# Optimization experiments

Hardware: AMD Instinct MI355X
Metric: run time of the kernel (lower is better)

Reference implementation:

```python
import jax, jax.numpy as jnp
import numpy as np

_J6 = jnp.array([[0, 0, 0, 0, 0, 1], [0, 0, 0, 0, -1, 0], [0, 0, 0, 1, 0, 0],
                 [0, 0, 1, 0, 0, 0], [0, -1, 0, 0, 0, 0], [1, 0, 0, 0, 0, 0]], dtype=jnp.float32)
_PAIRS4 = [(0, 1), (0, 2), (0, 3), (1, 2), (1, 3), (2, 3)]


def exterior(p1, p2):
    # p1, p2: (B,T,H,4) -> (B,T,H,6) normalized Pluecker line coordinates
    parts = [p1[..., i] * p2[..., j] - p1[..., j] * p2[..., i] for i, j in _PAIRS4]
    L = jnp.stack(parts, axis=-1)
    n = jnp.sqrt(jnp.sum(L * L, axis=-1, keepdims=True))
    return L / jnp.maximum(n, 1e-12)


def setup_inputs() -> dict:
    D, H = 1024, 16
    B, T = 2, 2048
    key = jax.random.key(0)
    ks = jax.random.split(key, 16)
    s = 0.02
    return {
        'x': jax.random.normal(ks[0], (B, T, D), dtype=jnp.float32),
        'qkv_w': jax.random.normal(ks[1], (D, 3 * D), dtype=jnp.float32) * s,
        'qkv_b': jnp.zeros((3 * D,), dtype=jnp.float32),
        'w1_write': jax.random.normal(ks[2], (D, 4 * H), dtype=jnp.float32) * s,
        'w2_write': jax.random.normal(ks[3], (D, 4 * H), dtype=jnp.float32) * s,
        'w1_read': jax.random.normal(ks[4], (D, 4 * H), dtype=jnp.float32) * s,
        'w2_read': jax.random.normal(ks[5], (D, 4 * H), dtype=jnp.float32) * s,
        'geo_w': jax.random.normal(ks[6], (D, D), dtype=jnp.float32) * s,
        'geo_b': jnp.zeros((D,), dtype=jnp.float32),
        'gate_w': jax.random.normal(ks[7], (D, H), dtype=jnp.float32) * s,
        'gate_b': jnp.zeros((H,), dtype=jnp.float32),
        'inc_scale': jnp.ones((H,), dtype=jnp.float32),
        'out_w': jax.random.normal(ks[8], (D, D), dtype=jnp.float32) * s,
        'out_b': jnp.zeros((D,), dtype=jnp.float32),
    }


def reference(x, qkv_w, qkv_b, w1_write, w2_write, w1_read, w2_read,
              geo_w, geo_b, gate_w, gate_b, inc_scale, out_w, out_b):
    B, T, D = x.shape
    H = inc_scale.shape[0]
    dh = D // H
    scale = dh ** -0.5

    qkv = (x @ qkv_w + qkv_b).reshape(B, T, 3, H, dh)
    qkv = jnp.transpose(qkv, (2, 0, 3, 1, 4))  # (3,B,H,T,dh)
    q, k, v = qkv[0], qkv[1], qkv[2]

    std_logits = jnp.einsum('bhqd,bhkd->bhqk', q, k) * scale

    x_prev = jnp.concatenate([jnp.zeros((B, 1, D), dtype=x.dtype), x[:, :-1]], axis=1)
    w1 = (x_prev @ w1_write).reshape(B, T, H, 4)
    w2 = (x @ w2_write).reshape(B, T, H, 4)
    write_lines = exterior(w1, w2)  # (B,T,H,6)
    r1 = (x @ w1_read).reshape(B, T, H, 4)
    r2 = (x @ w2_read).reshape(B, T, H, 4)
    read_lines = exterior(r1, r2)  # (B,T,H,6)

    J_write = jnp.einsum('bthi,ij->bthj', write_lines, _J6)  # (B,T,H,6)
    geo_logits = jnp.einsum('bqhi,bkhi->bhqk', read_lines, J_write)
    geo_logits = geo_logits * inc_scale.reshape(1, H, 1, 1)

    mask = jnp.triu(jnp.ones((T, T), dtype=bool), k=1)  # True above diagonal
    neg = jnp.float32(-jnp.inf)

    std_attn = jax.nn.softmax(jnp.where(mask, neg, std_logits), axis=-1)
    std_out = jnp.einsum('bhqk,bhkd->bqhd', std_attn, v).reshape(B, T, D)

    geo_attn = jax.nn.softmax(jnp.where(mask, neg, geo_logits), axis=-1)
    geo_v = (x @ geo_w + geo_b).reshape(B, T, H, dh)
    geo_out = jnp.einsum('bhqk,bkhd->bqhd', geo_attn, geo_v).reshape(B, T, D)

    gate = jax.nn.sigmoid(x @ gate_w + gate_b)  # (B,T,H)
    gate = jnp.mean(gate, axis=-1, keepdims=True)  # (B,T,1)

    combined = (1.0 - gate) * std_out + gate * geo_out
    return combined @ out_w + out_b
```

## Files before the change

### kernel.cpp

```cpp
#include <hip/hip_runtime.h>
#include <hip/hip_bf16.h>

#define Bc 2
#define Tc 2048
#define Dc 1024
#define Hc 16
#define Mc (Bc*Tc)
#define KB 32
#define NALL 4480
#define QSCALE 0.18033688056680776f
#define LOG2E  1.4426950408889634f

typedef __attribute__((ext_vector_type(8))) short bf16x8;
typedef __attribute__((ext_vector_type(4))) short bf16x4;
typedef __attribute__((ext_vector_type(4))) float fx4;

__device__ __forceinline__ short f2bf(float f) {
  __hip_bfloat16 h = __float2bfloat16(f);
  return *reinterpret_cast<short*>(&h);
}
__device__ __forceinline__ float bf2f(short s) {
  unsigned int u = ((unsigned int)(unsigned short)s) << 16;
  float f;
  __builtin_memcpy(&f, &u, 4);
  return f;
}

#define MFMA(a, b, c) __builtin_amdgcn_mfma_f32_16x16x32_bf16((a), (b), (c), 0, 0, 0)

#define GLD16(G, L) __builtin_amdgcn_global_load_lds( \
    (const __attribute__((address_space(1))) unsigned int*)(G), \
    (__attribute__((address_space(3))) unsigned int*)(L), 16, 0, 0)

__global__ __launch_bounds__(256) void f2b_k(const float* __restrict__ in,
                                             short* __restrict__ out) {
  const int i = blockIdx.x * 256 + threadIdx.x;
  const float4 v = ((const float4*)in)[i];
  bf16x4 o;
  o[0] = f2bf(v.x); o[1] = f2bf(v.y); o[2] = f2bf(v.z); o[3] = f2bf(v.w);
  ((bf16x4*)out)[i] = o;
}

__global__ void biasall_k(const float* __restrict__ qkv_b,
                          const float* __restrict__ geob,
                          const float* __restrict__ gateb,
                          float* __restrict__ ball) {
  const int n = blockIdx.x * 256 + threadIdx.x;
  if (n >= NALL) return;
  float v = 0.f;
  if (n < 1024)      v = qkv_b[n] * QSCALE;
  else if (n < 3072) v = qkv_b[n];
  else if (n < 4096) v = geob[n - 3072];
  else if (n >= 4352 && n < 4368) v = gateb[n - 4352];
  ball[n] = v;
}

__global__ __launch_bounds__(256) void tconv_all_k(
    const float* __restrict__ qkv_w, const float* __restrict__ geow,
    const float* __restrict__ w1w, const float* __restrict__ w2w,
    const float* __restrict__ w1r, const float* __restrict__ w2r,
    const float* __restrict__ gatew, short* __restrict__ wtall)
{
  __shared__ float tile[32][33];
  const int n0 = blockIdx.x * 32, k0 = blockIdx.y * 32;
  const int tx = threadIdx.x & 31, ty = threadIdx.x >> 5;
  const int n = n0 + tx;
  const float* src = nullptr; int ln = 0, sN = 0;
  if (n < 3072)      { src = qkv_w; ln = n;        sN = 3072; }
  else if (n < 4096) { src = geow;  ln = n - 3072; sN = 1024; }
  else if (n < 4160) { src = w1w;   ln = n - 4096; sN = 64; }
  else if (n < 4224) { src = w2w;   ln = n - 4160; sN = 64; }
  else if (n < 4288) { src = w1r;   ln = n - 4224; sN = 64; }
  else if (n < 4352) { src = w2r;   ln = n - 4288; sN = 64; }
  else if (n < 4368) { src = gatew; ln = n - 4352; sN = 16; }
  #pragma unroll
  for (int i = 0; i < 4; i++)
    tile[ty * 4 + i][tx] = src ? src[(size_t)(k0 + ty * 4 + i) * sN + ln] : 0.f;
  __syncthreads();
  #pragma unroll
  for (int i = 0; i < 4; i++) {
    const int nn = n0 + ty * 4 + i;
    const float s = (nn < 1024) ? QSCALE : 1.f;
    wtall[(size_t)nn * 1024 + k0 + tx] = f2bf(tile[tx][ty * 4 + i] * s);
  }
}

__global__ __launch_bounds__(256) void tconv_k(const float* __restrict__ W,
                                               short* __restrict__ Wt,
                                               int K, int N) {
  __shared__ float tile[32][33];
  const int k0 = blockIdx.y * 32, n0 = blockIdx.x * 32;
  const int tx = threadIdx.x & 31, ty = threadIdx.x >> 5;
  #pragma unroll
  for (int i = 0; i < 4; i++)
    tile[ty * 4 + i][tx] = W[(size_t)(k0 + ty * 4 + i) * N + n0 + tx];
  __syncthreads();
  #pragma unroll
  for (int i = 0; i < 4; i++)
    Wt[(size_t)(n0 + ty * 4 + i) * K + k0 + tx] = f2bf(tile[tx][ty * 4 + i]);
}

template<bool BF16_OUT>
__global__ __launch_bounds__(256) void gemm_mfma_k(
    const short* __restrict__ A, const short* __restrict__ Bt,
    const float* __restrict__ bias, void* __restrict__ Cv,
    int M, int N, int K)
{
  __shared__ short As[128][32];
  __shared__ short Bs[128][32];
  const int m0 = blockIdx.y * 128, n0 = blockIdx.x * 128;
  const int tid = threadIdx.x;
  const int wave = tid >> 6, lane = tid & 63;
  const int l15 = lane & 15, lg = lane >> 4;
  const int wm = wave >> 1, wn = wave & 1;
  const int srow = lane >> 2;
  const int schk = (lane & 3) * 8;

  const size_t aBase = (size_t)(m0 + wave * 16 + srow) * K + schk;
  const size_t bBase = (size_t)(n0 + wave * 16 + srow) * K + schk;

  fx4 acc[4][4] = {};

  for (int k0 = 0; k0 < K; k0 += 32) {
    __syncthreads();
    GLD16(&A[aBase + k0],              &As[wave * 16][0]);
    GLD16(&A[aBase + (size_t)64 * K + k0], &As[64 + wave * 16][0]);
    GLD16(&Bt[bBase + k0],             &Bs[wave * 16][0]);
    GLD16(&Bt[bBase + (size_t)64 * K + k0], &Bs[64 + wave * 16][0]);
    __syncthreads();
    bf16x8 af[4], bf[4];
    #pragma unroll
    for (int i = 0; i < 4; i++) {
      af[i] = *(const bf16x8*)&As[wm * 64 + i * 16 + l15][8 * lg];
      bf[i] = *(const bf16x8*)&Bs[wn * 64 + i * 16 + l15][8 * lg];
    }
    #pragma unroll
    for (int i = 0; i < 4; i++)
      #pragma unroll
      for (int j = 0; j < 4; j++)
        acc[i][j] = MFMA(af[i], bf[j], acc[i][j]);
  }

  #pragma unroll
  for (int i = 0; i < 4; i++)
    #pragma unroll
    for (int j = 0; j < 4; j++) {
      const int n = n0 + wn * 64 + j * 16 + l15;
      const float bv = bias ? bias[n] : 0.f;
      #pragma unroll
      for (int rg = 0; rg < 4; rg++) {
        const int m = m0 + wm * 64 + i * 16 + lg * 4 + rg;
        const float v = acc[i][j][rg] + bv;
        if constexpr (BF16_OUT)
          ((short*)Cv)[(size_t)m * N + n] = f2bf(v);
        else
          ((float*)Cv)[(size_t)m * N + n] = v;
      }
    }
}

__global__ __launch_bounds__(256) void vgt_k(const short* __restrict__ allb,
                                             short* __restrict__ vgt) {
  const int t0 = blockIdx.x * 64;
  const int bh = blockIdx.y;
  const int path = blockIdx.z;
  const int b = bh >> 4, h = bh & 15;
  __shared__ short tile[64][66];
  const int tt = threadIdx.x >> 2;
  const int dc = (threadIdx.x & 3) * 16;
  const size_t src = (size_t)(b * Tc + t0 + tt) * NALL + (path ? 3072 : 2048) + h * 64 + dc;
  *(bf16x8*)&tile[tt][dc]     = *(const bf16x8*)&allb[src];
  *(bf16x8*)&tile[tt][dc + 8] = *(const bf16x8*)&allb[src + 8];
  __syncthreads();
  const int dd = threadIdx.x >> 2;
  const int tc = (threadIdx.x & 3) * 16;
  bf16x8 o0, o1;
  #pragma unroll
  for (int j = 0; j < 8; j++) { o0[j] = tile[tc + j][dd]; o1[j] = tile[tc + 8 + j][dd]; }
  const size_t dst = ((size_t)(path * 32 + bh) * 64 + dd) * Tc + t0 + tc;
  *(bf16x8*)&vgt[dst]     = o0;
  *(bf16x8*)&vgt[dst + 8] = o1;
}

__device__ __forceinline__ void exterior6(const float a[4], const float c[4], float L[6]) {
  L[0] = a[0]*c[1] - a[1]*c[0];
  L[1] = a[0]*c[2] - a[2]*c[0];
  L[2] = a[0]*c[3] - a[3]*c[0];
  L[3] = a[1]*c[2] - a[2]*c[1];
  L[4] = a[1]*c[3] - a[3]*c[1];
  L[5] = a[2]*c[3] - a[3]*c[2];
}

__device__ __forceinline__ void load4bf(const short* p, float o[4]) {
  const bf16x4 v = *(const bf16x4*)p;
  o[0] = bf2f(v[0]); o[1] = bf2f(v[1]); o[2] = bf2f(v[2]); o[3] = bf2f(v[3]);
}

__global__ void lines_k(const short* __restrict__ allb,
                        const float* __restrict__ incs,
                        short* __restrict__ JWb, short* __restrict__ RLb)
{
  const int idx = blockIdx.x * 256 + threadIdx.x;
  if (idx >= Bc * Tc * Hc) return;
  const int h = idx & 15;
  const int t = (idx >> 4) & (Tc - 1);
  const int b = idx >> 15;
  const size_t row = (size_t)b * Tc + t;
  const size_t lrow = ((size_t)(b * Hc + h) * Tc + t) * 8;

  float a[4] = {0.f, 0.f, 0.f, 0.f};
  float c[4];
  load4bf(&allb[row * NALL + 4160 + h * 4], c);
  if (t > 0) load4bf(&allb[(row - 1) * NALL + 4096 + h * 4], a);

  float L[6];
  exterior6(a, c, L);
  float n = sqrtf(L[0]*L[0] + L[1]*L[1] + L[2]*L[2] + L[3]*L[3] + L[4]*L[4] + L[5]*L[5]);
  float inv = 1.f / fmaxf(n, 1e-12f);
  const float s = incs[h] * LOG2E;
  bf16x8 jw;
  jw[0] = f2bf( L[5] * inv * s);
  jw[1] = f2bf(-L[4] * inv * s);
  jw[2] = f2bf( L[3] * inv * s);
  jw[3] = f2bf( L[2] * inv * s);
  jw[4] = f2bf(-L[1] * inv * s);
  jw[5] = f2bf( L[0] * inv * s);
  jw[6] = 0; jw[7] = 0;
  *(bf16x8*)&JWb[lrow] = jw;

  load4bf(&allb[row * NALL + 4224 + h * 4], a);
  load4bf(&allb[row * NALL + 4288 + h * 4], c);
  exterior6(a, c, L);
  n = sqrtf(L[0]*L[0] + L[1]*L[1] + L[2]*L[2] + L[3]*L[3] + L[4]*L[4] + L[5]*L[5]);
  inv = 1.f / fmaxf(n, 1e-12f);
  bf16x8 rl;
  #pragma unroll
  for (int i = 0; i < 6; i++) rl[i] = f2bf(L[i] * inv);
  rl[6] = 0; rl[7] = 0;
  *(bf16x8*)&RLb[lrow] = rl;
}

__global__ void gate_k(const short* __restrict__ allb, float* __restrict__ gate) {
  const int idx = blockIdx.x * 256 + threadIdx.x;
  if (idx >= Mc) return;
  float ssum = 0.f;
  #pragma unroll
  for (int hh = 0; hh < 16; hh++) {
    const float v = bf2f(allb[(size_t)idx * NALL + 4352 + hh]);
    ssum += 1.f / (1.f + __expf(-v));
  }
  gate[idx] = ssum * (1.f / 16.f);
}

#define LOADKJ(K0, k00, k01, k10, k11, j0, j1) { \
  const size_t rb0 = (size_t)(b * Tc + (K0) + l15) * NALL + 1024 + h * 64; \
  const size_t rb1 = rb0 + (size_t)16 * NALL; \
  k00 = *(const bf16x8*)&allb[rb0 + lg * 8]; \
  k01 = *(const bf16x8*)&allb[rb0 + 32 + lg * 8]; \
  k10 = *(const bf16x8*)&allb[rb1 + lg * 8]; \
  k11 = *(const bf16x8*)&allb[rb1 + 32 + lg * 8]; \
  j0 = z8; j1 = z8; \
  if (lg == 0) { \
    j0 = *(const bf16x8*)&JWb[(size_t)(bh * Tc + (K0) + l15) * 8]; \
    j1 = *(const bf16x8*)&JWb[(size_t)(bh * Tc + (K0) + 16 + l15) * 8]; \
  } }

#define GSTAGE(CUR, K0) { \
  GLD16(&vgt[vgbase + (K0)], &Vt[CUR][wave * 16][0]); \
  GLD16(&vgt[vgbase + GOFF + (K0)], &Gt[CUR][wave * 16][0]); }

#define COMPUTE(K0, CUR, k00, k01, k10, k11, j0, j1) \
  if ((K0) <= qhi) { \
    const fx4 z = {0.f, 0.f, 0.f, 0.f}; \
    fx4 sS0, sS1, sG0, sG1; \
    __builtin_amdgcn_s_setprio(1); \
    sS0 = MFMA(qf0, k00, z); sS0 = MFMA(qf1, k01, sS0); \
    sS1 = MFMA(qf0, k10, z); sS1 = MFMA(qf1, k11, sS1); \
    sG0 = MFMA(rlf, j0, z);  sG1 = MFMA(rlf, j1, z); \
    __builtin_amdgcn_s_setprio(0); \
    if ((K0) + KB - 1 > q0 + wave * 16) { \
      const int kg0 = (K0) + l15, kg1 = (K0) + 16 + l15; \
      _Pragma("unroll") for (int r = 0; r < 4; r++) { \
        const int qg = q0 + wave * 16 + lg * 4 + r; \
        if (kg0 > qg) { sS0[r] = -1e30f; sG0[r] = -1e30f; } \
        if (kg1 > qg) { sS1[r] = -1e30f; sG1[r] = -1e30f; } \
      } } \
    _Pragma("unroll") for (int r = 0; r < 4; r++) { \
      const int ql = lg * 4 + r; \
      const float p0 = exp2f(sS0[r]); const float p1 = exp2f(sS1[r]); \
      lpS[r] += p0 + p1; \
      Ps[wave][ql][l15] = f2bf(p0); Ps[wave][ql][16 + l15] = f2bf(p1); \
      const float g0 = exp2f(sG0[r]); const float g1 = exp2f(sG1[r]); \
      lpG[r] += g0 + g1; \
      Pg[wave][ql][l15] = f2bf(g0); Pg[wave][ql][16 + l15] = f2bf(g1); \
    } \
    const bf16x8 pa  = *(const bf16x8*)&Ps[wave][l15][8 * lg]; \
    const bf16x8 pga = *(const bf16x8*)&Pg[wave][l15][8 * lg]; \
    __builtin_amdgcn_s_setprio(1); \
    _Pragma("unroll") for (int dt = 0; dt < 4; dt++) { \
      const int dV = dt * 16 + l15; \
      accS[dt] = MFMA(pa,  *(const bf16x8*)&Vt[CUR][dV][rpos], accS[dt]); \
      accG[dt] = MFMA(pga, *(const bf16x8*)&Gt[CUR][dV][rpos], accG[dt]); \
    } \
    __builtin_amdgcn_s_setprio(0); \
  }

__global__ __launch_bounds__(256) void attn5_k(
    const short* __restrict__ allb,
    const short* __restrict__ vgt,
    const short* __restrict__ RLb,
    const short* __restrict__ JWb,
    const float* __restrict__ gate,
    short* __restrict__ combb)
{
  const int orig = blockIdx.x;
  const int xcd  = orig & 7;
  const int idx  = orig >> 3;
  const int pairIdx = idx & 15;
  const int bh   = xcd + 8 * (idx >> 4);
  const int b = bh >> 4, h = bh & 15;
  const int tid = threadIdx.x;
  const int wave = tid >> 6;
  const int lane = tid & 63;
  const int l15 = lane & 15;
  const int lg  = lane >> 4;

  __shared__ short Vt[2][64][32];
  __shared__ short Gt[2][64][32];
  __shared__ short Ps[4][16][40];
  __shared__ short Pg[4][16][40];

  const bf16x8 z8 = {0, 0, 0, 0, 0, 0, 0, 0};

  const int srow = wave * 16 + (lane >> 2);
  const int schunk = ((lane & 3) - (srow >> 1)) & 3;
  const size_t vgbase = ((size_t)bh * 64 + srow) * Tc + schunk * 8;
  const size_t GOFF = (size_t)32 * 64 * Tc;
  const int rpos = ((lg + (l15 >> 1)) & 3) * 8;

  for (int half = 0; half < 2; half++) {
    const int qt = half ? (31 - pairIdx) : pairIdx;
    const int q0 = qt * 64;
    const int nkt = 2 * qt + 2;
    const int qrow = wave * 16 + l15;
    const int qhi = q0 + wave * 16 + 15;

    const size_t qrb = (size_t)(b * Tc + q0 + qrow) * NALL + h * 64;
    const bf16x8 qf0 = *(const bf16x8*)&allb[qrb + lg * 8];
    const bf16x8 qf1 = *(const bf16x8*)&allb[qrb + 32 + lg * 8];
    bf16x8 rlf = z8;
    if (lg == 0) rlf = *(const bf16x8*)&RLb[(size_t)(bh * Tc + q0 + qrow) * 8];

    fx4 accS[4] = {}, accG[4] = {};
    float lpS[4] = {0.f, 0.f, 0.f, 0.f};
    float lpG[4] = {0.f, 0.f, 0.f, 0.f};

    bf16x8 kA00, kA01, kA10, kA11, jA0, jA1;
    bf16x8 kB00, kB01, kB10, kB11, jB0, jB1;

    GSTAGE(0, 0);
    LOADKJ(0, kA00, kA01, kA10, kA11, jA0, jA1);
    __syncthreads();

    for (int kt = 0; kt < nkt; kt += 2) {
      GSTAGE(1, (kt + 1) * KB);
      LOADKJ((kt + 1) * KB, kB00, kB01, kB10, kB11, jB0, jB1);
      COMPUTE(kt * KB, 0, kA00, kA01, kA10, kA11, jA0, jA1);
      __syncthreads();
      if (kt + 2 < nkt) {
        GSTAGE(0, (kt + 2) * KB);
        LOADKJ((kt + 2) * KB, kA00, kA01, kA10, kA11, jA0, jA1);
      }
      COMPUTE((kt + 1) * KB, 1, kB00, kB01, kB10, kB11, jB0, jB1);
      __syncthreads();
    }

    #pragma unroll
    for (int r = 0; r < 4; r++) {
      float ls = lpS[r];
      ls += __shfl_xor(ls, 1); ls += __shfl_xor(ls, 2);
      ls += __shfl_xor(ls, 4); ls += __shfl_xor(ls, 8);
      float lgeo = lpG[r];
      lgeo += __shfl_xor(lgeo, 1); lgeo += __shfl_xor(lgeo, 2);
      lgeo += __shfl_xor(lgeo, 4); lgeo += __shfl_xor(lgeo, 8);
      const int qg = q0 + wave * 16 + lg * 4 + r;
      const float gt = gate[(size_t)b * Tc + qg];
      const float invS = (1.f - gt) / ls;
      const float invG = gt / lgeo;
      #pragma unroll
      for (int dt = 0; dt < 4; dt++) {
        const float o = accS[dt][r] * invS + accG[dt][r] * invG;
        combb[(size_t)(b * Tc + qg) * 1024 + h * 64 + dt * 16 + l15] = f2bf(o);
      }
    }
  }
}

extern "C" void kernel_launch(void* const* d_in, const int* in_sizes, int n_in,
                              void* d_out, int out_size, void* d_ws, size_t ws_size,
                              hipStream_t stream) {
  (void)in_sizes; (void)n_in; (void)out_size; (void)ws_size;
  const float* x     = (const float*)d_in[0];
  const float* qkv_w = (const float*)d_in[1];
  const float* qkv_b = (const float*)d_in[2];
  const float* w1w   = (const float*)d_in[3];
  const float* w2w   = (const float*)d_in[4];
  const float* w1r   = (const float*)d_in[5];
  const float* w2r   = (const float*)d_in[6];
  const float* geow  = (const float*)d_in[7];
  const float* geob  = (const float*)d_in[8];
  const float* gatew = (const float*)d_in[9];
  const float* gateb = (const float*)d_in[10];
  const float* incs  = (const float*)d_in[11];
  const float* outw  = (const float*)d_in[12];
  const float* outb  = (const float*)d_in[13];
  float* out = (float*)d_out;

  char* p = (char*)d_ws;
  short* xb    = (short*)p;  p += (size_t)4096 * 1024 * 2;
  short* wtall = (short*)p;  p += (size_t)NALL * 1024 * 2;
  short* allb  = (short*)p;  p += (size_t)4096 * NALL * 2;
  short* vgt   = (short*)p;  p += (size_t)2 * 32 * 64 * Tc * 2;
  short* combb = (short*)p;  p += (size_t)4096 * 1024 * 2;
  short* wtout = (short*)p;  p += (size_t)1024 * 1024 * 2;
  short* JWb   = (short*)p;  p += (size_t)32 * 2048 * 8 * 2;
  short* RLb   = (short*)p;  p += (size_t)32 * 2048 * 8 * 2;
  float* ball  = (float*)p;  p += (size_t)NALL * 4;
  float* gatev = (float*)p;  p += (size_t)4096 * 4;

  const dim3 blk(256);

  f2b_k<<<dim3(4096), blk, 0, stream>>>(x, xb);
  biasall_k<<<dim3((NALL + 255) / 256), blk, 0, stream>>>(qkv_b, geob, gateb, ball);
  tconv_all_k<<<dim3(NALL / 32, 32), blk, 0, stream>>>(qkv_w, geow, w1w, w2w, w1r, w2r, gatew, wtall);
  tconv_k<<<dim3(32, 32), blk, 0, stream>>>(outw, wtout, 1024, 1024);

  gemm_mfma_k<true><<<dim3(NALL / 128, 32), blk, 0, stream>>>(xb, wtall, ball, allb, 4096, NALL, 1024);

  vgt_k<<<dim3(Tc / 64, 32, 2), blk, 0, stream>>>(allb, vgt);
  lines_k<<<dim3((Bc * Tc * Hc + 255) / 256), blk, 0, stream>>>(allb, incs, JWb, RLb);
  gate_k<<<dim3((Mc + 255) / 256), blk, 0, stream>>>(allb, gatev);

  attn5_k<<<dim3(512), blk, 0, stream>>>(allb, vgt, RLb, JWb, gatev, combb);

  gemm_mfma_k<false><<<dim3(8, 32), blk, 0, stream>>>(combb, wtout, outb, (void*)out, 4096, 1024, 1024);
}
```

Before: 217.4 us.

## Split fused standard/geometric attention into separate blocks and add combine kernel

The attention kernel now assigns the standard-softmax path and the geometric-line path to different thread blocks, doubling the grid from 512 to 1024 blocks. Each block keeps only one accumulator set and one LDS staging buffer, which lowers register and shared-memory pressure. Each path writes its gated, normalized partial output to a scratch buffer that reuses the input-conversion workspace. A new elementwise kernel then sums the two partials. The cost is an extra launch plus extra global traffic for the partial outputs. The geometric blocks also do much less work than the standard ones, so load across blocks is uneven.

Measured after the change: 235.5 us. 1.08x slower.

```diff
diff --git a/kernel.cpp b/kernel.cpp
--- a/kernel.cpp
+++ b/kernel.cpp
@@ -252,72 +252,71 @@
   gate[idx] = ssum * (1.f / 16.f);
 }
 
-#define LOADKJ(K0, k00, k01, k10, k11, j0, j1) { \
-  const size_t rb0 = (size_t)(b * Tc + (K0) + l15) * NALL + 1024 + h * 64; \
-  const size_t rb1 = rb0 + (size_t)16 * NALL; \
-  k00 = *(const bf16x8*)&allb[rb0 + lg * 8]; \
-  k01 = *(const bf16x8*)&allb[rb0 + 32 + lg * 8]; \
-  k10 = *(const bf16x8*)&allb[rb1 + lg * 8]; \
-  k11 = *(const bf16x8*)&allb[rb1 + 32 + lg * 8]; \
-  j0 = z8; j1 = z8; \
-  if (lg == 0) { \
-    j0 = *(const bf16x8*)&JWb[(size_t)(bh * Tc + (K0) + l15) * 8]; \
-    j1 = *(const bf16x8*)&JWb[(size_t)(bh * Tc + (K0) + 16 + l15) * 8]; \
+#define LOADOPS(K0, o00, o01, o10, o11) { \
+  if (path == 0) { \
+    const size_t rb0 = (size_t)(b * Tc + (K0) + l15) * NALL + 1024 + h * 64; \
+    const size_t rb1 = rb0 + (size_t)16 * NALL; \
+    o00 = *(const bf16x8*)&allb[rb0 + lg * 8]; \
+    o01 = *(const bf16x8*)&allb[rb0 + 32 + lg * 8]; \
+    o10 = *(const bf16x8*)&allb[rb1 + lg * 8]; \
+    o11 = *(const bf16x8*)&allb[rb1 + 32 + lg * 8]; \
+  } else if (lg == 0) { \
+    o00 = *(const bf16x8*)&JWb[(size_t)(bh * Tc + (K0) + l15) * 8]; \
+    o10 = *(const bf16x8*)&JWb[(size_t)(bh * Tc + (K0) + 16 + l15) * 8]; \
   } }
 
-#define GSTAGE(CUR, K0) { \
-  GLD16(&vgt[vgbase + (K0)], &Vt[CUR][wave * 16][0]); \
-  GLD16(&vgt[vgbase + GOFF + (K0)], &Gt[CUR][wave * 16][0]); }
-
-#define COMPUTE(K0, CUR, k00, k01, k10, k11, j0, j1) \
+#define GSTAGE(CUR, K0) GLD16(&vgsrc[vgbase + (K0)], &Vt[CUR][wave * 16][0])
+
+#define COMPUTE(K0, CUR, o00, o01, o10, o11) \
   if ((K0) <= qhi) { \
     const fx4 z = {0.f, 0.f, 0.f, 0.f}; \
-    fx4 sS0, sS1, sG0, sG1; \
+    fx4 s0, s1; \
     __builtin_amdgcn_s_setprio(1); \
-    sS0 = MFMA(qf0, k00, z); sS0 = MFMA(qf1, k01, sS0); \
-    sS1 = MFMA(qf0, k10, z); sS1 = MFMA(qf1, k11, sS1); \
-    sG0 = MFMA(rlf, j0, z);  sG1 = MFMA(rlf, j1, z); \
+    if (path == 0) { \
+      s0 = MFMA(qf0, o00, z); s0 = MFMA(qf1, o01, s0); \
+      s1 = MFMA(qf0, o10, z); s1 = MFMA(qf1, o11, s1); \
+    } else { \
+      s0 = MFMA(rlf, o00, z); \
+      s1 = MFMA(rlf, o10, z); \
+    } \
     __builtin_amdgcn_s_setprio(0); \
     if ((K0) + KB - 1 > q0 + wave * 16) { \
       const int kg0 = (K0) + l15, kg1 = (K0) + 16 + l15; \
       _Pragma("unroll") for (int r = 0; r < 4; r++) { \
         const int qg = q0 + wave * 16 + lg * 4 + r; \
-        if (kg0 > qg) { sS0[r] = -1e30f; sG0[r] = -1e30f; } \
-        if (kg1 > qg) { sS1[r] = -1e30f; sG1[r] = -1e30f; } \
+        if (kg0 > qg) s0[r] = -1e30f; \
+        if (kg1 > qg) s1[r] = -1e30f; \
       } } \
     _Pragma("unroll") for (int r = 0; r < 4; r++) { \
       const int ql = lg * 4 + r; \
-      const float p0 = exp2f(sS0[r]); const float p1 = exp2f(sS1[r]); \
-      lpS[r] += p0 + p1; \
+      const float p0 = exp2f(s0[r]); const float p1 = exp2f(s1[r]); \
+      lp[r] += p0 + p1; \
       Ps[wave][ql][l15] = f2bf(p0); Ps[wave][ql][16 + l15] = f2bf(p1); \
-      const float g0 = exp2f(sG0[r]); const float g1 = exp2f(sG1[r]); \
-      lpG[r] += g0 + g1; \
-      Pg[wave][ql][l15] = f2bf(g0); Pg[wave][ql][16 + l15] = f2bf(g1); \
     } \
-    const bf16x8 pa  = *(const bf16x8*)&Ps[wave][l15][8 * lg]; \
-    const bf16x8 pga = *(const bf16x8*)&Pg[wave][l15][8 * lg]; \
+    const bf16x8 pa = *(const bf16x8*)&Ps[wave][l15][8 * lg]; \
     __builtin_amdgcn_s_setprio(1); \
     _Pragma("unroll") for (int dt = 0; dt < 4; dt++) { \
       const int dV = dt * 16 + l15; \
-      accS[dt] = MFMA(pa,  *(const bf16x8*)&Vt[CUR][dV][rpos], accS[dt]); \
-      accG[dt] = MFMA(pga, *(const bf16x8*)&Gt[CUR][dV][rpos], accG[dt]); \
+      acc[dt] = MFMA(pa, *(const bf16x8*)&Vt[CUR][dV][rpos], acc[dt]); \
     } \
     __builtin_amdgcn_s_setprio(0); \
   }
 
-__global__ __launch_bounds__(256) void attn5_k(
+__global__ __launch_bounds__(256) void attn6_k(
     const short* __restrict__ allb,
     const short* __restrict__ vgt,
     const short* __restrict__ RLb,
     const short* __restrict__ JWb,
     const float* __restrict__ gate,
-    short* __restrict__ combb)
+    short* __restrict__ outPb)
 {
   const int orig = blockIdx.x;
   const int xcd  = orig & 7;
-  const int idx  = orig >> 3;
-  const int pairIdx = idx & 15;
-  const int bh   = xcd + 8 * (idx >> 4);
+  const int rest = orig >> 3;
+  const int bh   = xcd + 8 * (rest >> 5);
+  const int inner = rest & 31;
+  const int pairIdx = inner & 15;
+  const int path = inner >> 4;
   const int b = bh >> 4, h = bh & 15;
   const int tid = threadIdx.x;
   const int wave = tid >> 6;
@@ -326,16 +325,14 @@
   const int lg  = lane >> 4;
 
   __shared__ short Vt[2][64][32];
-  __shared__ short Gt[2][64][32];
   __shared__ short Ps[4][16][40];
-  __shared__ short Pg[4][16][40];
 
   const bf16x8 z8 = {0, 0, 0, 0, 0, 0, 0, 0};
 
   const int srow = wave * 16 + (lane >> 2);
   const int schunk = ((lane & 3) - (srow >> 1)) & 3;
   const size_t vgbase = ((size_t)bh * 64 + srow) * Tc + schunk * 8;
-  const size_t GOFF = (size_t)32 * 64 * Tc;
+  const short* vgsrc = vgt + (size_t)path * 32 * 64 * Tc;
   const int rpos = ((lg + (l15 >> 1)) & 3) * 8;
 
   for (int half = 0; half < 2; half++) {
@@ -345,55 +342,63 @@
     const int qrow = wave * 16 + l15;
     const int qhi = q0 + wave * 16 + 15;
 
-    const size_t qrb = (size_t)(b * Tc + q0 + qrow) * NALL + h * 64;
-    const bf16x8 qf0 = *(const bf16x8*)&allb[qrb + lg * 8];
-    const bf16x8 qf1 = *(const bf16x8*)&allb[qrb + 32 + lg * 8];
-    bf16x8 rlf = z8;
-    if (lg == 0) rlf = *(const bf16x8*)&RLb[(size_t)(bh * Tc + q0 + qrow) * 8];
-
-    fx4 accS[4] = {}, accG[4] = {};
-    float lpS[4] = {0.f, 0.f, 0.f, 0.f};
-    float lpG[4] = {0.f, 0.f, 0.f, 0.f};
-
-    bf16x8 kA00, kA01, kA10, kA11, jA0, jA1;
-    bf16x8 kB00, kB01, kB10, kB11, jB0, jB1;
+    bf16x8 qf0 = z8, qf1 = z8, rlf = z8;
+    if (path == 0) {
+      const size_t qrb = (size_t)(b * Tc + q0 + qrow) * NALL + h * 64;
+      qf0 = *(const bf16x8*)&allb[qrb + lg * 8];
+      qf1 = *(const bf16x8*)&allb[qrb + 32 + lg * 8];
+    } else if (lg == 0) {
+      rlf = *(const bf16x8*)&RLb[(size_t)(bh * Tc + q0 + qrow) * 8];
+    }
+
+    fx4 acc[4] = {};
+    float lp[4] = {0.f, 0.f, 0.f, 0.f};
+
+    bf16x8 oA00 = z8, oA01 = z8, oA10 = z8, oA11 = z8;
+    bf16x8 oB00 = z8, oB01 = z8, oB10 = z8, oB11 = z8;
 
     GSTAGE(0, 0);
-    LOADKJ(0, kA00, kA01, kA10, kA11, jA0, jA1);
+    LOADOPS(0, oA00, oA01, oA10, oA11);
     __syncthreads();
 
     for (int kt = 0; kt < nkt; kt += 2) {
       GSTAGE(1, (kt + 1) * KB);
-      LOADKJ((kt + 1) * KB, kB00, kB01, kB10, kB11, jB0, jB1);
-      COMPUTE(kt * KB, 0, kA00, kA01, kA10, kA11, jA0, jA1);
+      LOADOPS((kt + 1) * KB, oB00, oB01, oB10, oB11);
+      COMPUTE(kt * KB, 0, oA00, oA01, oA10, oA11);
       __syncthreads();
       if (kt + 2 < nkt) {
         GSTAGE(0, (kt + 2) * KB);
-        LOADKJ((kt + 2) * KB, kA00, kA01, kA10, kA11, jA0, jA1);
+        LOADOPS((kt + 2) * KB, oA00, oA01, oA10, oA11);
       }
-      COMPUTE((kt + 1) * KB, 1, kB00, kB01, kB10, kB11, jB0, jB1);
+      COMPUTE((kt + 1) * KB, 1, oB00, oB01, oB10, oB11);
       __syncthreads();
     }
 
     #pragma unroll
     for (int r = 0; r < 4; r++) {
-      float ls = lpS[r];
+      float ls = lp[r];
       ls += __shfl_xor(ls, 1); ls += __shfl_xor(ls, 2);
       ls += __shfl_xor(ls, 4); ls += __shfl_xor(ls, 8);
-      float lgeo = lpG[r];
-      lgeo += __shfl_xor(lgeo, 1); lgeo += __shfl_xor(lgeo, 2);
-      lgeo += __shfl_xor(lgeo, 4); lgeo += __shfl_xor(lgeo, 8);
       const int qg = q0 + wave * 16 + lg * 4 + r;
       const float gt = gate[(size_t)b * Tc + qg];
-      const float invS = (1.f - gt) / ls;
-      const float invG = gt / lgeo;
+      const float fac = (path == 0 ? (1.f - gt) : gt) / ls;
+      short* op = &outPb[((size_t)path * Mc + b * Tc + qg) * 1024 + h * 64];
       #pragma unroll
-      for (int dt = 0; dt < 4; dt++) {
-        const float o = accS[dt][r] * invS + accG[dt][r] * invG;
-        combb[(size_t)(b * Tc + qg) * 1024 + h * 64 + dt * 16 + l15] = f2bf(o);
-      }
+      for (int dt = 0; dt < 4; dt++)
+        op[dt * 16 + l15] = f2bf(acc[dt][r] * fac);
     }
   }
+}
+
+__global__ __launch_bounds__(256) void combine_k(const short* __restrict__ outPb,
+                                                 short* __restrict__ combb) {
+  const size_t i = ((size_t)blockIdx.x * 256 + threadIdx.x) * 8;
+  const bf16x8 va = *(const bf16x8*)&outPb[i];
+  const bf16x8 vb = *(const bf16x8*)&outPb[(size_t)Mc * 1024 + i];
+  bf16x8 vo;
+  #pragma unroll
+  for (int j = 0; j < 8; j++) vo[j] = f2bf(bf2f(va[j]) + bf2f(vb[j]));
+  *(bf16x8*)&combb[i] = vo;
 }
 
 extern "C" void kernel_launch(void* const* d_in, const int* in_sizes, int n_in,
@@ -427,6 +432,7 @@
   short* RLb   = (short*)p;  p += (size_t)32 * 2048 * 8 * 2;
   float* ball  = (float*)p;  p += (size_t)NALL * 4;
   float* gatev = (float*)p;  p += (size_t)4096 * 4;
+  short* outPb = xb;
 
   const dim3 blk(256);
 
@@ -441,7 +447,8 @@
   lines_k<<<dim3((Bc * Tc * Hc + 255) / 256), blk, 0, stream>>>(allb, incs, JWb, RLb);
   gate_k<<<dim3((Mc + 255) / 256), blk, 0, stream>>>(allb, gatev);
 
-  attn5_k<<<dim3(512), blk, 0, stream>>>(allb, vgt, RLb, JWb, gatev, combb);
+  attn6_k<<<dim3(1024), blk, 0, stream>>>(allb, vgt, RLb, JWb, gatev, outPb);
+  combine_k<<<dim3(2048), blk, 0, stream>>>(outPb, combb);
 
   gemm_mfma_k<false><<<dim3(8, 32), blk, 0, stream>>>(combb, wtout, outb, (void*)out, 4096, 1024, 1024);
 }
```
